# Optimization experiments

Measured on AMD Instinct MI355X. Metric: run time of the kernel, lower is better.

The kernel has to match this reference:

```python
import jax, jax.numpy as jnp
import numpy as np

B, NV, NRINGS, NDIRS, C, F = 2, 20000, 8, 8, 16, 16


def setup_inputs() -> dict:
    key = jax.random.key(0)
    ks = jax.random.split(key, 7)
    y = jax.random.normal(ks[0], (B, NV, NDIRS, C), jnp.float32)
    contributors = jax.random.randint(ks[1], (NV, NRINGS, NDIRS, 3), 0, NV, dtype=jnp.int32)
    weights_bary = jax.random.uniform(ks[2], (NV, NRINGS, NDIRS, 3), jnp.float32)
    angles = jax.random.randint(ks[3], (NV, NRINGS, NDIRS, 3), 0, NDIRS, dtype=jnp.int32)
    kernel = jax.random.normal(ks[4], (NRINGS, NDIRS, C, F), jnp.float32) * 0.05
    center_kernel = jax.random.normal(ks[5], (C, F), jnp.float32) * 0.05
    bias = jnp.zeros((F,), jnp.float32)
    return {"y": y, "contributors": contributors, "weights_bary": weights_bary,
            "angles": angles, "kernel": kernel, "center_kernel": center_kernel, "bias": bias}


def reference(y, contributors, weights_bary, angles, kernel, center_kernel, bias):
    # y: (B, nv, ndirs, C); tables: (nv, nrings, ndirs, 3)
    b, nv, ndirs, nch = y.shape
    nfilters = kernel.shape[-1]
    nrings = contributors.shape[1]

    # window_interpolation_sync: gather 3 contributor vertices per window bin,
    # with the direction axis re-indexed per-contributor (radial sync), then
    # barycentric-weighted sum.  Flatten (vertex, dir) into one gather index.
    idx = contributors * ndirs + angles                 # (nv, nrings, ndirs, 3)
    y_flat = y.reshape(b, nv * ndirs, nch)
    gathered = y_flat[:, idx, :]                        # (B, nv, nrings, ndirs, 3, C)
    z = jnp.einsum('bvrdjc,vrdj->bvrdc', gathered, weights_bary)  # (B, nv, nrings, ndirs, C)

    # gcnn_conv: circular pad over dirs then VALID conv with (nrings, ndirs) kernel
    zr = z.reshape(b * nv, nrings, ndirs, nch)
    zr = jnp.concatenate([zr, zr[:, :, :-1, :]], axis=2)  # width 2*ndirs-1
    conv = jax.lax.conv_general_dilated(
        zr, kernel, window_strides=(1, 1), padding='VALID',
        dimension_numbers=('NHWC', 'HWIO', 'NHWC'))       # (B*nv, 1, ndirs, F)
    conv = conv.reshape(b, nv, ndirs, nfilters)

    out = conv + jnp.einsum('bvdc,cf->bvdf', y, center_kernel) + bias
    out = jax.nn.relu(out)
    return jnp.max(out, axis=2)                          # take_max over directions -> (B, nv, F)
```

## Files before the change

kernel.cpp:

```cpp
#include <hip/hip_runtime.h>

typedef unsigned short u16;
typedef __attribute__((ext_vector_type(4))) unsigned int u32x4;
typedef __attribute__((ext_vector_type(4))) float f32x4;
typedef __attribute__((ext_vector_type(8))) __bf16 bf16x8;

constexpr int BATCH = 2;
constexpr int NV    = 20000;
constexpr int ND    = 8;
constexpr int CH    = 16;
constexpr int NF    = 16;
constexpr int NVD   = NV * ND;
constexpr int NCHUNK = 36;
constexpr int MTOT  = BATCH * NV;
constexpr int BSTR  = 40;

constexpr size_t Y16_OFF_B = 0;
constexpr size_t K2C_OFF_B = 10240000;

__device__ __forceinline__ u16 f2bf(float x) {
    unsigned int u = __float_as_uint(x);
    unsigned int r = (u + 0x7fffu + ((u >> 16) & 1u)) >> 16;
    return (u16)r;
}
__device__ __forceinline__ unsigned int pack2bf(float a, float b) {
    return (unsigned int)f2bf(a) | ((unsigned int)f2bf(b) << 16);
}

__global__ __launch_bounds__(256) void prep(const float* __restrict__ y,
                                            u16* __restrict__ y16) {
    int tid = blockIdx.x * 256 + threadIdx.x;
    const float4* src = (const float4*)(y + (size_t)tid * 16);
    float4 v0 = src[0], v1 = src[1], v2 = src[2], v3 = src[3];
    u32x4 lo = {pack2bf(v0.x, v0.y), pack2bf(v0.z, v0.w), pack2bf(v1.x, v1.y), pack2bf(v1.z, v1.w)};
    u32x4 hi = {pack2bf(v2.x, v2.y), pack2bf(v2.z, v2.w), pack2bf(v3.x, v3.y), pack2bf(v3.z, v3.w)};
    u16* yd = y16 + (size_t)tid * 16;
    *(u32x4*)(yd)     = lo;
    *(u32x4*)(yd + 8) = hi;
}

__global__ __launch_bounds__(256) void k2_build(const float* __restrict__ kern,
                                                const float* __restrict__ ck,
                                                u16* __restrict__ k2c) {
    int e = blockIdx.x * 256 + threadIdx.x;
    int i = e & 4095;
    int kc = e >> 12;
    int n = i >> 5, kk = i & 31;
    int k = kc * 32 + kk;
    int w = n >> 4, f = n & 15;
    float val;
    if (k < 1024) {
        int r = k >> 7, dd = (k >> 4) & 7, c = k & 15;
        int d = (dd - w) & 7;
        val = kern[((r * 8 + d) * 16 + c) * 16 + f];
    } else {
        int ke = k - 1024;
        int d = ke >> 4, c = ke & 15;
        val = (d == w) ? ck[c * 16 + f] : 0.f;
    }
    k2c[e] = f2bf(val);
}

__global__ __launch_bounds__(256) void fused_gather_gemm(const u16* __restrict__ y16,
                                                         const int* __restrict__ contrib,
                                                         const float* __restrict__ wbary,
                                                         const int* __restrict__ angles,
                                                         const u16* __restrict__ k2c,
                                                         const float* __restrict__ bias,
                                                         float* __restrict__ out) {
    __shared__ __align__(16) u16 Bb[2][128 * BSTR];
    const int t = threadIdx.x;
    const int w = t >> 6, lane = t & 63;
    const int lrow = lane & 15, lq = lane >> 4;
    const int s_p = lq >> 1;
    const int h8  = (lq & 1) * 8;
    const int m0 = blockIdx.x * 64;
    const int arow = m0 + w * 16 + lrow;
    const int b_p = (arow >= NV);
    const int v_p = arow - b_p * NV;
    const u16* __restrict__ yb = y16 + (size_t)b_p * NVD * CH + h8;
    const int mb0 = v_p * 192 + s_p * 3;
    const int sn = t >> 1, sh = (t & 1) * 16;

    int   ce0, ce1, ce2, ae0, ae1, ae2;  float we0, we1, we2;
    int   co0, co1, co2, ao0, ao1, ao2;  float wo0, wo1, wo2;
    u32x4 ge0, ge1, ge2;  float ve0, ve1, ve2;
    u32x4 go0, go1, go2;  float vo0, vo1, vo2;
    u32x4 bne0, bne1, bno0, bno1;

    f32x4 acc[8];
    #pragma unroll
    for (int nt = 0; nt < 8; ++nt) acc[nt] = (f32x4){0.f, 0.f, 0.f, 0.f};

#define META_ISSUE(S, KC_) { const int o_ = mb0 + (KC_) * 6;                       \
    c##S##0 = contrib[o_]; c##S##1 = contrib[o_ + 1]; c##S##2 = contrib[o_ + 2];   \
    a##S##0 = angles[o_];  a##S##1 = angles[o_ + 1];  a##S##2 = angles[o_ + 2];    \
    w##S##0 = wbary[o_];   w##S##1 = wbary[o_ + 1];   w##S##2 = wbary[o_ + 2]; }

#define G_ISSUE(S, KC_) {                                                          \
    if ((KC_) < 32) {                                                              \
        g##S##0 = *(const u32x4*)(yb + (size_t)((unsigned)c##S##0 * 128u +         \
                                                (unsigned)a##S##0 * 16u));         \
        g##S##1 = *(const u32x4*)(yb + (size_t)((unsigned)c##S##1 * 128u +         \
                                                (unsigned)a##S##1 * 16u));         \
        g##S##2 = *(const u32x4*)(yb + (size_t)((unsigned)c##S##2 * 128u +         \
                                                (unsigned)a##S##2 * 16u));         \
        v##S##0 = w##S##0; v##S##1 = w##S##1; v##S##2 = w##S##2;                   \
    } else {                                                                       \
        g##S##0 = *(const u32x4*)(yb + (size_t)((unsigned)v_p * 128u +             \
                                      (unsigned)(2 * ((KC_) - 32) + s_p) * 16u));  \
    } }

#define COMBINE(S, KC_, A_) {                                                      \
    if ((KC_) < 32) {                                                              \
        float ac_[8];                                                              \
        _Pragma("unroll") for (int x_ = 0; x_ < 8; ++x_) ac_[x_] = 0.f;            \
        _Pragma("unroll")                                                          \
        for (int q_ = 0; q_ < 4; ++q_) {                                           \
            unsigned u0_ = g##S##0[q_], u1_ = g##S##1[q_], u2_ = g##S##2[q_];      \
            ac_[2 * q_]     += v##S##0 * __uint_as_float(u0_ << 16);               \
            ac_[2 * q_ + 1] += v##S##0 * __uint_as_float(u0_ & 0xffff0000u);       \
            ac_[2 * q_]     += v##S##1 * __uint_as_float(u1_ << 16);               \
            ac_[2 * q_ + 1] += v##S##1 * __uint_as_float(u1_ & 0xffff0000u);       \
            ac_[2 * q_]     += v##S##2 * __uint_as_float(u2_ << 16);               \
            ac_[2 * q_ + 1] += v##S##2 * __uint_as_float(u2_ & 0xffff0000u);       \
        }                                                                          \
        u32x4 o_;                                                                  \
        _Pragma("unroll") for (int q_ = 0; q_ < 4; ++q_)                           \
            o_[q_] = pack2bf(ac_[2 * q_], ac_[2 * q_ + 1]);                        \
        A_ = *(bf16x8*)&o_;                                                        \
    } else { u32x4 o_ = g##S##0; A_ = *(bf16x8*)&o_; } }

    META_ISSUE(e, 0); META_ISSUE(o, 1);
    {
        const u32x4* src = (const u32x4*)(k2c + (size_t)0 * 4096 + sn * 32 + sh);
        u32x4 b0 = src[0], b1 = src[1];
        u16* dst = &Bb[0][sn * BSTR + sh];
        *(u32x4*)(dst)     = b0;
        *(u32x4*)(dst + 8) = b1;
    }
    G_ISSUE(e, 0); META_ISSUE(e, 2);
    G_ISSUE(o, 1);
    {
        const u32x4* src = (const u32x4*)(k2c + (size_t)1 * 4096 + sn * 32 + sh);
        bno0 = src[0]; bno1 = src[1];
    }

    for (int p = 0; p < 18; ++p) {
        const int k0 = 2 * p, k1 = 2 * p + 1;

        __syncthreads();
        if (k0 + 2 < NCHUNK) {
            const u32x4* src = (const u32x4*)(k2c + (size_t)(k0 + 2) * 4096 + sn * 32 + sh);
            bne0 = src[0]; bne1 = src[1];
        }
        bf16x8 aev;
        COMBINE(e, k0, aev);
        if (k0 + 2 < NCHUNK) G_ISSUE(e, k0 + 2);
        if (k0 + 3 < 32)     META_ISSUE(o, k0 + 3);
        {
            bf16x8 bf[8];
            #pragma unroll
            for (int nt = 0; nt < 8; ++nt)
                bf[nt] = *(const bf16x8*)(&Bb[0][(nt * 16 + lrow) * BSTR + lq * 8]);
            #pragma unroll
            for (int nt = 0; nt < 8; ++nt)
                acc[nt] = __builtin_amdgcn_mfma_f32_16x16x32_bf16(aev, bf[nt], acc[nt], 0, 0, 0);
        }
        {
            u16* dst = &Bb[1][sn * BSTR + sh];
            *(u32x4*)(dst)     = bno0;
            *(u32x4*)(dst + 8) = bno1;
        }

        __syncthreads();
        if (k1 + 2 < NCHUNK) {
            const u32x4* src = (const u32x4*)(k2c + (size_t)(k1 + 2) * 4096 + sn * 32 + sh);
            bno0 = src[0]; bno1 = src[1];
        }
        bf16x8 aov;
        COMBINE(o, k1, aov);
        if (k1 + 2 < NCHUNK) G_ISSUE(o, k1 + 2);
        if (k1 + 3 < 32)     META_ISSUE(e, k1 + 3);
        {
            bf16x8 bf[8];
            #pragma unroll
            for (int nt = 0; nt < 8; ++nt)
                bf[nt] = *(const bf16x8*)(&Bb[1][(nt * 16 + lrow) * BSTR + lq * 8]);
            #pragma unroll
            for (int nt = 0; nt < 8; ++nt)
                acc[nt] = __builtin_amdgcn_mfma_f32_16x16x32_bf16(aov, bf[nt], acc[nt], 0, 0, 0);
        }
        if (k1 + 1 < NCHUNK) {
            u16* dst = &Bb[0][sn * BSTR + sh];
            *(u32x4*)(dst)     = bne0;
            *(u32x4*)(dst + 8) = bne1;
        }
    }
#undef META_ISSUE
#undef G_ISSUE
#undef COMBINE

    const float bb = bias[lrow];
    #pragma unroll
    for (int reg = 0; reg < 4; ++reg) {
        float m = 0.f;
        #pragma unroll
        for (int nt = 0; nt < 8; ++nt) m = fmaxf(m, acc[nt][reg] + bb);
        out[((size_t)(m0 + w * 16 + lq * 4 + reg)) * NF + lrow] = m;
    }
}

extern "C" void kernel_launch(void* const* d_in, const int* in_sizes, int n_in,
                              void* d_out, int out_size, void* d_ws, size_t ws_size,
                              hipStream_t stream) {
    const float* y      = (const float*)d_in[0];
    const int*   contrib= (const int*)d_in[1];
    const float* wbary  = (const float*)d_in[2];
    const int*   angles = (const int*)d_in[3];
    const float* kern   = (const float*)d_in[4];
    const float* ck     = (const float*)d_in[5];
    const float* bias   = (const float*)d_in[6];
    float* out = (float*)d_out;

    u16* y16 = (u16*)((char*)d_ws + Y16_OFF_B);
    u16* k2c = (u16*)((char*)d_ws + K2C_OFF_B);

    prep<<<1250, 256, 0, stream>>>(y, y16);
    k2_build<<<(NCHUNK * 4096) / 256, 256, 0, stream>>>(kern, ck, k2c);
    fused_gather_gemm<<<MTOT / 64, 256, 0, stream>>>(y16, contrib, wbary, angles,
                                                     k2c, bias, out);
}
```

Baseline: 239.5 us.

## Repack gather metadata, read B directly from global, XCD-aware tile mapping

Merges the two prep kernels into one launch and adds a third prep pass that packs contributor/angle offsets and barycentric weights into 32-byte records per (vertex, sub-row, chunk), so the main kernel does two vector loads instead of nine scalar ones. The main kernel drops the LDS double-buffered B tile and its barriers, loading B fragments straight from global/L2. The software pipeline deepens to a three-stage rotation. Blocks are remapped so each XCD group works on one batch, sharing the metadata stream for a vertex tile. The prep pass now rewrites the whole metadata table every call, adding extra memory traffic.

```diff
diff --git a/kernel.cpp b/kernel.cpp
--- a/kernel.cpp
+++ b/kernel.cpp
@@ -5,18 +5,20 @@
 typedef __attribute__((ext_vector_type(4))) float f32x4;
 typedef __attribute__((ext_vector_type(8))) __bf16 bf16x8;
 
-constexpr int BATCH = 2;
 constexpr int NV    = 20000;
 constexpr int ND    = 8;
 constexpr int CH    = 16;
 constexpr int NF    = 16;
 constexpr int NVD   = NV * ND;
 constexpr int NCHUNK = 36;
-constexpr int MTOT  = BATCH * NV;
-constexpr int BSTR  = 40;
-
-constexpr size_t Y16_OFF_B = 0;
-constexpr size_t K2C_OFF_B = 10240000;
+constexpr int TPB   = 313;
+constexpr int PREP_BLOCKS = 1250;
+constexpr int K2_BLOCKS   = 576;
+constexpr int MREC_BLOCKS = 5000;
+
+constexpr size_t Y16_OFF_B  = 0;
+constexpr size_t K2C_OFF_B  = 10240000;
+constexpr size_t MREC_OFF_B = 10534912;
 
 __device__ __forceinline__ u16 f2bf(float x) {
     unsigned int u = __float_as_uint(x);
@@ -27,85 +29,102 @@
     return (unsigned int)f2bf(a) | ((unsigned int)f2bf(b) << 16);
 }
 
-__global__ __launch_bounds__(256) void prep(const float* __restrict__ y,
-                                            u16* __restrict__ y16) {
-    int tid = blockIdx.x * 256 + threadIdx.x;
-    const float4* src = (const float4*)(y + (size_t)tid * 16);
-    float4 v0 = src[0], v1 = src[1], v2 = src[2], v3 = src[3];
-    u32x4 lo = {pack2bf(v0.x, v0.y), pack2bf(v0.z, v0.w), pack2bf(v1.x, v1.y), pack2bf(v1.z, v1.w)};
-    u32x4 hi = {pack2bf(v2.x, v2.y), pack2bf(v2.z, v2.w), pack2bf(v3.x, v3.y), pack2bf(v3.z, v3.w)};
-    u16* yd = y16 + (size_t)tid * 16;
-    *(u32x4*)(yd)     = lo;
-    *(u32x4*)(yd + 8) = hi;
-}
-
-__global__ __launch_bounds__(256) void k2_build(const float* __restrict__ kern,
-                                                const float* __restrict__ ck,
-                                                u16* __restrict__ k2c) {
-    int e = blockIdx.x * 256 + threadIdx.x;
-    int i = e & 4095;
-    int kc = e >> 12;
-    int n = i >> 5, kk = i & 31;
-    int k = kc * 32 + kk;
-    int w = n >> 4, f = n & 15;
-    float val;
-    if (k < 1024) {
-        int r = k >> 7, dd = (k >> 4) & 7, c = k & 15;
-        int d = (dd - w) & 7;
-        val = kern[((r * 8 + d) * 16 + c) * 16 + f];
+__global__ __launch_bounds__(256) void prep_k2(const float* __restrict__ y,
+                                               u16* __restrict__ y16,
+                                               const float* __restrict__ kern,
+                                               const float* __restrict__ ck,
+                                               u16* __restrict__ k2c,
+                                               const int* __restrict__ contrib,
+                                               const int* __restrict__ angles,
+                                               const float* __restrict__ wbary,
+                                               unsigned* __restrict__ mrec) {
+    int bid = blockIdx.x;
+    if (bid < PREP_BLOCKS) {
+        int tid = bid * 256 + threadIdx.x;
+        const float4* src = (const float4*)(y + (size_t)tid * 16);
+        float4 v0 = src[0], v1 = src[1], v2 = src[2], v3 = src[3];
+        u32x4 lo = {pack2bf(v0.x, v0.y), pack2bf(v0.z, v0.w), pack2bf(v1.x, v1.y), pack2bf(v1.z, v1.w)};
+        u32x4 hi = {pack2bf(v2.x, v2.y), pack2bf(v2.z, v2.w), pack2bf(v3.x, v3.y), pack2bf(v3.z, v3.w)};
+        u16* yd = y16 + (size_t)tid * 16;
+        *(u32x4*)(yd)     = lo;
+        *(u32x4*)(yd + 8) = hi;
+    } else if (bid < PREP_BLOCKS + K2_BLOCKS) {
+        int e = (bid - PREP_BLOCKS) * 256 + threadIdx.x;
+        int i = e & 4095;
+        int kc = e >> 12;
+        int n = i >> 5, kk = i & 31;
+        int k = kc * 32 + kk;
+        int w = n >> 4, f = n & 15;
+        float val;
+        if (k < 1024) {
+            int r = k >> 7, dd = (k >> 4) & 7, c = k & 15;
+            int d = (dd - w) & 7;
+            val = kern[((r * 8 + d) * 16 + c) * 16 + f];
+        } else {
+            int ke = k - 1024;
+            int d = ke >> 4, c = ke & 15;
+            val = (d == w) ? ck[c * 16 + f] : 0.f;
+        }
+        k2c[e] = f2bf(val);
     } else {
-        int ke = k - 1024;
-        int d = ke >> 4, c = ke & 15;
-        val = (d == w) ? ck[c * 16 + f] : 0.f;
+        int tid = (bid - (PREP_BLOCKS + K2_BLOCKS)) * 256 + threadIdx.x;
+        int v = tid >> 6, rd = tid & 63;
+        int kc = rd >> 1, sp = rd & 1;
+        const int*   cp = contrib + (size_t)tid * 3;
+        const int*   ap = angles  + (size_t)tid * 3;
+        const float* wp = wbary   + (size_t)tid * 3;
+        u32x4 r0;
+        r0[0] = (unsigned)(cp[0] * 128 + ap[0] * 16);
+        r0[1] = (unsigned)(cp[1] * 128 + ap[1] * 16);
+        r0[2] = (unsigned)(cp[2] * 128 + ap[2] * 16);
+        r0[3] = __float_as_uint(wp[0]);
+        float2 r1 = {wp[1], wp[2]};
+        unsigned* dst = mrec + ((size_t)(v * 2 + sp) * 32 + kc) * 8;
+        *(u32x4*)(dst)      = r0;
+        *(float2*)(dst + 4) = r1;
     }
-    k2c[e] = f2bf(val);
-}
-
-__global__ __launch_bounds__(256) void fused_gather_gemm(const u16* __restrict__ y16,
-                                                         const int* __restrict__ contrib,
-                                                         const float* __restrict__ wbary,
-                                                         const int* __restrict__ angles,
-                                                         const u16* __restrict__ k2c,
-                                                         const float* __restrict__ bias,
-                                                         float* __restrict__ out) {
-    __shared__ __align__(16) u16 Bb[2][128 * BSTR];
+}
+
+__global__ __launch_bounds__(256, 4) void fused_gather_gemm(const u16* __restrict__ y16,
+                                                            const unsigned* __restrict__ mrec,
+                                                            const u16* __restrict__ k2c,
+                                                            const float* __restrict__ bias,
+                                                            float* __restrict__ out) {
+    const int bid = blockIdx.x;
+    const int xcd = bid & 7;
+    const int g   = xcd >> 2;
+    const int tile = (bid >> 3) * 4 + (xcd & 3);
+    if (tile >= TPB) return;
     const int t = threadIdx.x;
     const int w = t >> 6, lane = t & 63;
     const int lrow = lane & 15, lq = lane >> 4;
     const int s_p = lq >> 1;
     const int h8  = (lq & 1) * 8;
-    const int m0 = blockIdx.x * 64;
-    const int arow = m0 + w * 16 + lrow;
-    const int b_p = (arow >= NV);
-    const int v_p = arow - b_p * NV;
-    const u16* __restrict__ yb = y16 + (size_t)b_p * NVD * CH + h8;
-    const int mb0 = v_p * 192 + s_p * 3;
-    const int sn = t >> 1, sh = (t & 1) * 16;
-
-    int   ce0, ce1, ce2, ae0, ae1, ae2;  float we0, we1, we2;
-    int   co0, co1, co2, ao0, ao1, ao2;  float wo0, wo1, wo2;
-    u32x4 ge0, ge1, ge2;  float ve0, ve1, ve2;
-    u32x4 go0, go1, go2;  float vo0, vo1, vo2;
-    u32x4 bne0, bne1, bno0, bno1;
+    const int rb  = tile * 64 + w * 16 + lrow;
+    const int v_p = rb < NV ? rb : NV - 1;
+    const u16* __restrict__ yb = y16 + (size_t)g * NVD * CH + h8;
+    const unsigned* __restrict__ mb = mrec + (size_t)(v_p * 2 + s_p) * 256;
+    const u16* __restrict__ kb = k2c + lrow * 32 + lq * 8;
+
+    u32x4 miA, miB, miC;
+    float2 mwA, mwB, mwC;
+    u32x4 gA0, gA1, gA2, gB0, gB1, gB2, gC0, gC1, gC2;
+    float vA0, vA1, vA2, vB0, vB1, vB2, vC0, vC1, vC2;
 
     f32x4 acc[8];
     #pragma unroll
     for (int nt = 0; nt < 8; ++nt) acc[nt] = (f32x4){0.f, 0.f, 0.f, 0.f};
 
-#define META_ISSUE(S, KC_) { const int o_ = mb0 + (KC_) * 6;                       \
-    c##S##0 = contrib[o_]; c##S##1 = contrib[o_ + 1]; c##S##2 = contrib[o_ + 2];   \
-    a##S##0 = angles[o_];  a##S##1 = angles[o_ + 1];  a##S##2 = angles[o_ + 2];    \
-    w##S##0 = wbary[o_];   w##S##1 = wbary[o_ + 1];   w##S##2 = wbary[o_ + 2]; }
+#define META_ISSUE(S, KC_) { mi##S = *(const u32x4*)(mb + (KC_) * 8);              \
+                             mw##S = *(const float2*)(mb + (KC_) * 8 + 4); }
 
 #define G_ISSUE(S, KC_) {                                                          \
     if ((KC_) < 32) {                                                              \
-        g##S##0 = *(const u32x4*)(yb + (size_t)((unsigned)c##S##0 * 128u +         \
-                                                (unsigned)a##S##0 * 16u));         \
-        g##S##1 = *(const u32x4*)(yb + (size_t)((unsigned)c##S##1 * 128u +         \
-                                                (unsigned)a##S##1 * 16u));         \
-        g##S##2 = *(const u32x4*)(yb + (size_t)((unsigned)c##S##2 * 128u +         \
-                                                (unsigned)a##S##2 * 16u));         \
-        v##S##0 = w##S##0; v##S##1 = w##S##1; v##S##2 = w##S##2;                   \
+        g##S##0 = *(const u32x4*)(yb + mi##S[0]);                                  \
+        g##S##1 = *(const u32x4*)(yb + mi##S[1]);                                  \
+        g##S##2 = *(const u32x4*)(yb + mi##S[2]);                                  \
+        v##S##0 = __uint_as_float(mi##S[3]);                                       \
+        v##S##1 = mw##S.x; v##S##2 = mw##S.y;                                      \
     } else {                                                                       \
         g##S##0 = *(const u32x4*)(yb + (size_t)((unsigned)v_p * 128u +             \
                                       (unsigned)(2 * ((KC_) - 32) + s_p) * 16u));  \
@@ -131,83 +150,59 @@
         A_ = *(bf16x8*)&o_;                                                        \
     } else { u32x4 o_ = g##S##0; A_ = *(bf16x8*)&o_; } }
 
-    META_ISSUE(e, 0); META_ISSUE(o, 1);
-    {
-        const u32x4* src = (const u32x4*)(k2c + (size_t)0 * 4096 + sn * 32 + sh);
-        u32x4 b0 = src[0], b1 = src[1];
-        u16* dst = &Bb[0][sn * BSTR + sh];
-        *(u32x4*)(dst)     = b0;
-        *(u32x4*)(dst + 8) = b1;
-    }
-    G_ISSUE(e, 0); META_ISSUE(e, 2);
-    G_ISSUE(o, 1);
-    {
-        const u32x4* src = (const u32x4*)(k2c + (size_t)1 * 4096 + sn * 32 + sh);
-        bno0 = src[0]; bno1 = src[1];
-    }
-
-    for (int p = 0; p < 18; ++p) {
-        const int k0 = 2 * p, k1 = 2 * p + 1;
-
-        __syncthreads();
-        if (k0 + 2 < NCHUNK) {
-            const u32x4* src = (const u32x4*)(k2c + (size_t)(k0 + 2) * 4096 + sn * 32 + sh);
-            bne0 = src[0]; bne1 = src[1];
-        }
-        bf16x8 aev;
-        COMBINE(e, k0, aev);
-        if (k0 + 2 < NCHUNK) G_ISSUE(e, k0 + 2);
-        if (k0 + 3 < 32)     META_ISSUE(o, k0 + 3);
-        {
-            bf16x8 bf[8];
-            #pragma unroll
-            for (int nt = 0; nt < 8; ++nt)
-                bf[nt] = *(const bf16x8*)(&Bb[0][(nt * 16 + lrow) * BSTR + lq * 8]);
-            #pragma unroll
-            for (int nt = 0; nt < 8; ++nt)
-                acc[nt] = __builtin_amdgcn_mfma_f32_16x16x32_bf16(aev, bf[nt], acc[nt], 0, 0, 0);
-        }
-        {
-            u16* dst = &Bb[1][sn * BSTR + sh];
-            *(u32x4*)(dst)     = bno0;
-            *(u32x4*)(dst + 8) = bno1;
-        }
-
-        __syncthreads();
-        if (k1 + 2 < NCHUNK) {
-            const u32x4* src = (const u32x4*)(k2c + (size_t)(k1 + 2) * 4096 + sn * 32 + sh);
-            bno0 = src[0]; bno1 = src[1];
-        }
-        bf16x8 aov;
-        COMBINE(o, k1, aov);
-        if (k1 + 2 < NCHUNK) G_ISSUE(o, k1 + 2);
-        if (k1 + 3 < 32)     META_ISSUE(e, k1 + 3);
-        {
-            bf16x8 bf[8];
-            #pragma unroll
-            for (int nt = 0; nt < 8; ++nt)
-                bf[nt] = *(const bf16x8*)(&Bb[1][(nt * 16 + lrow) * BSTR + lq * 8]);
-            #pragma unroll
-            for (int nt = 0; nt < 8; ++nt)
-                acc[nt] = __builtin_amdgcn_mfma_f32_16x16x32_bf16(aov, bf[nt], acc[nt], 0, 0, 0);
-        }
-        if (k1 + 1 < NCHUNK) {
-            u16* dst = &Bb[0][sn * BSTR + sh];
-            *(u32x4*)(dst)     = bne0;
-            *(u32x4*)(dst + 8) = bne1;
-        }
+#define CHUNK(S, KC_) {                                                            \
+    bf16x8 av_;                                                                    \
+    COMBINE(S, KC_, av_);                                                          \
+    if ((KC_) + 3 < NCHUNK) G_ISSUE(S, (KC_) + 3)                                  \
+    if ((KC_) + 6 < 32)     META_ISSUE(S, (KC_) + 6)                               \
+    const u16* kb_ = kb + (size_t)(KC_) * 4096;                                    \
+    {   bf16x8 b0_ = *(const bf16x8*)(kb_);                                        \
+        bf16x8 b1_ = *(const bf16x8*)(kb_ + 512);                                  \
+        bf16x8 b2_ = *(const bf16x8*)(kb_ + 1024);                                 \
+        bf16x8 b3_ = *(const bf16x8*)(kb_ + 1536);                                 \
+        acc[0] = __builtin_amdgcn_mfma_f32_16x16x32_bf16(av_, b0_, acc[0], 0, 0, 0); \
+        acc[1] = __builtin_amdgcn_mfma_f32_16x16x32_bf16(av_, b1_, acc[1], 0, 0, 0); \
+        acc[2] = __builtin_amdgcn_mfma_f32_16x16x32_bf16(av_, b2_, acc[2], 0, 0, 0); \
+        acc[3] = __builtin_amdgcn_mfma_f32_16x16x32_bf16(av_, b3_, acc[3], 0, 0, 0); \
+    }                                                                              \
+    {   bf16x8 b4_ = *(const bf16x8*)(kb_ + 2048);                                 \
+        bf16x8 b5_ = *(const bf16x8*)(kb_ + 2560);                                 \
+        bf16x8 b6_ = *(const bf16x8*)(kb_ + 3072);                                 \
+        bf16x8 b7_ = *(const bf16x8*)(kb_ + 3584);                                 \
+        acc[4] = __builtin_amdgcn_mfma_f32_16x16x32_bf16(av_, b4_, acc[4], 0, 0, 0); \
+        acc[5] = __builtin_amdgcn_mfma_f32_16x16x32_bf16(av_, b5_, acc[5], 0, 0, 0); \
+        acc[6] = __builtin_amdgcn_mfma_f32_16x16x32_bf16(av_, b6_, acc[6], 0, 0, 0); \
+        acc[7] = __builtin_amdgcn_mfma_f32_16x16x32_bf16(av_, b7_, acc[7], 0, 0, 0); \
+    } }
+
+    META_ISSUE(A, 0)
+    META_ISSUE(B, 1)
+    META_ISSUE(C, 2)
+    G_ISSUE(A, 0) META_ISSUE(A, 3)
+    G_ISSUE(B, 1) META_ISSUE(B, 4)
+    G_ISSUE(C, 2) META_ISSUE(C, 5)
+
+    for (int p = 0; p < 12; ++p) {
+        const int base = 3 * p;
+        CHUNK(A, base)
+        CHUNK(B, base + 1)
+        CHUNK(C, base + 2)
     }
 #undef META_ISSUE
 #undef G_ISSUE
 #undef COMBINE
-
-    const float bb = bias[lrow];
-    #pragma unroll
-    for (int reg = 0; reg < 4; ++reg) {
-        float m = 0.f;
+#undef CHUNK
+
+    if (tile * 64 + w * 16 + lq * 4 < NV) {
+        const float bb = bias[lrow];
+        const int m0 = g * NV + tile * 64 + w * 16 + lq * 4;
         #pragma unroll
-        for (int nt = 0; nt < 8; ++nt) m = fmaxf(m, acc[nt][reg] + bb);
-        out[((size_t)(m0 + w * 16 + lq * 4 + reg)) * NF + lrow] = m;
+        for (int reg = 0; reg < 4; ++reg) {
+            float m = 0.f;
+            #pragma unroll
+            for (int nt = 0; nt < 8; ++nt) m = fmaxf(m, acc[nt][reg] + bb);
+            out[(size_t)(m0 + reg) * NF + lrow] = m;
+        }
     }
 }
 
@@ -223,11 +218,12 @@
     const float* bias   = (const float*)d_in[6];
     float* out = (float*)d_out;
 
-    u16* y16 = (u16*)((char*)d_ws + Y16_OFF_B);
-    u16* k2c = (u16*)((char*)d_ws + K2C_OFF_B);
-
-    prep<<<1250, 256, 0, stream>>>(y, y16);
-    k2_build<<<(NCHUNK * 4096) / 256, 256, 0, stream>>>(kern, ck, k2c);
-    fused_gather_gemm<<<MTOT / 64, 256, 0, stream>>>(y16, contrib, wbary, angles,
-                                                     k2c, bias, out);
-}
+    u16*      y16  = (u16*)((char*)d_ws + Y16_OFF_B);
+    u16*      k2c  = (u16*)((char*)d_ws + K2C_OFF_B);
+    unsigned* mrec = (unsigned*)((char*)d_ws + MREC_OFF_B);
+
+    prep_k2<<<PREP_BLOCKS + K2_BLOCKS + MREC_BLOCKS, 256, 0, stream>>>(
+        y, y16, kern, ck, k2c, contrib, angles, wbary, mrec);
+    fused_gather_gemm<<<((TPB + 3) / 4) * 8, 256, 0, stream>>>(
+        y16, mrec, k2c, bias, out);
+}
```

Result: slower. 289.7 us (+21.0%).
